# Kernel tuning notes

Hardware: AMD Instinct MI355X
Metric: run time of the kernel (lower is better)

Reference implementation:

```python
import jax, jax.numpy as jnp
import numpy as np

N = 50000
E = 1600000
IN = 128
HID = 128
OUT = 64
NL = 200000
NEG_SLOPE = 0.2


def _glorot(key, shape):
    fan_in, fan_out = shape[0], shape[-1]
    s = jnp.sqrt(6.0 / (fan_in + fan_out))
    return jax.random.uniform(key, shape, jnp.float32, -s, s)


def setup_inputs() -> dict:
    key = jax.random.key(0)
    ks = jax.random.split(key, 16)
    x = jax.random.normal(ks[0], (N, IN), jnp.float32)
    edge_index = jax.random.randint(ks[1], (2, E), 0, N, dtype=jnp.int32)
    edge_label_index = jax.random.randint(ks[2], (2, NL), 0, N, dtype=jnp.int32)
    return {
        "x": x,
        "edge_index": edge_index,
        "edge_label_index": edge_label_index,
        "W1": _glorot(ks[3], (IN, HID)),  "a1s": _glorot(ks[4], (HID,)),  "a1d": _glorot(ks[5], (HID,)),  "b1": jnp.zeros((HID,), jnp.float32),
        "W2": _glorot(ks[6], (HID, HID)), "a2s": _glorot(ks[7], (HID,)),  "a2d": _glorot(ks[8], (HID,)),  "b2": jnp.zeros((HID,), jnp.float32),
        "W3": _glorot(ks[9], (HID, HID)), "a3s": _glorot(ks[10], (HID,)), "a3d": _glorot(ks[11], (HID,)), "b3": jnp.zeros((HID,), jnp.float32),
        "W4": _glorot(ks[12], (HID, OUT)), "b4": jnp.zeros((OUT,), jnp.float32),
    }


def _add_self_loops(edge_index, n):
    loop = jnp.arange(n, dtype=edge_index.dtype)
    return jnp.concatenate([edge_index, jnp.stack([loop, loop])], axis=1)


def gat_conv(x, edge_index, W, a_s, a_d, b):
    """PyG GATConv, heads=1, add_self_loops=True: gather, LeakyReLU score,
    segment softmax over destination nodes, scatter-add aggregate."""
    n = x.shape[0]
    ei = _add_self_loops(edge_index, n)
    src, dst = ei[0], ei[1]
    h = x @ W                                    # [N, H]
    e = jax.nn.leaky_relu((h @ a_s)[src] + (h @ a_d)[dst], NEG_SLOPE)  # [E']
    m = jax.ops.segment_max(e, dst, num_segments=n)
    p = jnp.exp(e - m[dst])
    s = jax.ops.segment_sum(p, dst, num_segments=n)
    alpha = p / s[dst]                           # segment softmax
    out = jax.ops.segment_sum(h[src] * alpha[:, None], dst, num_segments=n)
    return out + b


def gcn_conv(x, edge_index, W, b):
    """PyG GCNConv: self-loops + symmetric degree normalization."""
    n = x.shape[0]
    ei = _add_self_loops(edge_index, n)
    src, dst = ei[0], ei[1]
    h = x @ W
    deg = jax.ops.segment_sum(jnp.ones(src.shape, h.dtype), dst, num_segments=n)
    dinv = jax.lax.rsqrt(deg)
    norm = dinv[src] * dinv[dst]                 # [E']
    out = jax.ops.segment_sum(h[src] * norm[:, None], dst, num_segments=n)
    return out + b


def reference(x, edge_index, edge_label_index,
              W1, a1s, a1d, b1, W2, a2s, a2d, b2,
              W3, a3s, a3d, b3, W4, b4):
    h = jax.nn.relu(gat_conv(x, edge_index, W1, a1s, a1d, b1))
    h = jax.nn.relu(gat_conv(h, edge_index, W2, a2s, a2d, b2))
    h = jax.nn.relu(gat_conv(h, edge_index, W3, a3s, a3d, b3))
    z = gcn_conv(h, edge_index, W4, b4)          # [N, OUT]
    # decode: dot product of endpoint embeddings -> link logits [NL]
    return (z[edge_label_index[0]] * z[edge_label_index[1]]).sum(axis=-1)
```

## Files before the change

### kernel.cpp

```cpp
#include <hip/hip_runtime.h>
#include <hip/hip_fp16.h>
#include <math.h>

#define NN   50000
#define NE   1600000
#define NLBL 200000
#define CAP  80
#define NEG  0.2f
#define NBK  196
#define CAPB 8800
#define CHK  4096
#define GBIN 391

typedef unsigned short u16;
typedef _Float16 half8 __attribute__((ext_vector_type(8)));
typedef float floatx4 __attribute__((ext_vector_type(4)));


__device__ void ph_bin(int blk, const int* __restrict__ ei,
                       int* __restrict__ gcnt, unsigned* __restrict__ bins) {
    __shared__ int cntL[NBK];
    __shared__ int offL[NBK];
    __shared__ int curL[NBK];
    __shared__ int curG[NBK];
    __shared__ unsigned stage[CHK];
    const int tid = threadIdx.x;
    const int e0 = blk * CHK + tid * 16;
    const bool act = (e0 + 15) < NE;

    unsigned pk[16];
    int bb[16];
    if (act) {
#pragma unroll
        for (int g = 0; g < 4; ++g) {
            int4 s4 = *(const int4*)&ei[e0 + g * 4];
            int4 d4 = *(const int4*)&ei[NE + e0 + g * 4];
            int sa[4] = {s4.x, s4.y, s4.z, s4.w};
            int da[4] = {d4.x, d4.y, d4.z, d4.w};
#pragma unroll
            for (int k = 0; k < 4; ++k) {
                int idx = g * 4 + k;
                bb[idx] = da[k] >> 8;
                pk[idx] = (unsigned)sa[k] | ((unsigned)(da[k] & 255) << 16)
                        | ((unsigned)bb[idx] << 24);
            }
        }
    }
    for (int i = tid; i < NBK; i += 256) cntL[i] = 0;
    __syncthreads();
    if (act) {
#pragma unroll
        for (int k = 0; k < 16; ++k) atomicAdd(&cntL[bb[k]], 1);
    }
    __syncthreads();
    if (tid < NBK) {
        int acc = 0;
        for (int i = 0; i < tid; ++i) acc += cntL[i];
        offL[tid] = acc;
        curL[tid] = acc;
    }
    __syncthreads();
    for (int i = tid; i < NBK; i += 256) curG[i] = atomicAdd(&gcnt[i], cntL[i]);
    __syncthreads();
    if (act) {
#pragma unroll
        for (int k = 0; k < 16; ++k) {
            int pos = atomicAdd(&curL[bb[k]], 1);
            stage[pos] = pk[k];
        }
    }
    __syncthreads();
    const int tot = offL[NBK - 1] + cntL[NBK - 1];
    for (int j = tid; j < tot; j += 256) {
        unsigned v = stage[j];
        int b = v >> 24;
        int lr = j - offL[b];
        bins[(size_t)b * CAPB + curG[b] + lr] = v & 0x00FFFFFFu;
    }
}

__global__ __launch_bounds__(256) void k_build(const unsigned* __restrict__ bins,
                                               const int* __restrict__ gcnt,
                                               int* __restrict__ cnt,
                                               u16* __restrict__ csr) {
    __shared__ u16 rows[256 * CAP];
    __shared__ int cur[256];
    const int b = blockIdx.x, tid = threadIdx.x;
    const int d0 = b << 8;
    const int nd = min(256, NN - d0);
    if (tid < nd) { cur[tid] = 1; rows[tid * CAP] = (u16)(d0 + tid); }
    __syncthreads();
    const int n = gcnt[b];
    for (int i = tid; i < n; i += 256) {
        unsigned v = bins[(size_t)b * CAPB + i];
        int s = v & 0xFFFF, dl = (v >> 16) & 0xFF;
        int pos = atomicAdd(&cur[dl], 1);
        if (pos < CAP) rows[dl * CAP + pos] = (u16)s;
    }
    __syncthreads();
    const unsigned* rw = (const unsigned*)rows;
    unsigned* cw = (unsigned*)(csr + (size_t)d0 * CAP);
    const int tot = nd * (CAP / 2);
    for (int i = tid; i < tot; i += 256) cw[i] = rw[i];
    if (tid < nd) cnt[d0 + tid] = cur[tid];
}


__global__ __launch_bounds__(256) void k_pre(const float* __restrict__ W1f,
                                             const float* __restrict__ W2f,
                                             const float* __restrict__ W3f,
                                             const float* __restrict__ W4f,
                                             half8* __restrict__ Wf1,
                                             half8* __restrict__ Wf2,
                                             half8* __restrict__ Wf3,
                                             half8* __restrict__ Wf4,
                                             int* __restrict__ gcnt) {
    if (blockIdx.x == 28) {
        int i = threadIdx.x;
        if (i < NBK) gcnt[i] = 0;
        return;
    }
    int e = blockIdx.x * 256 + threadIdx.x;
    const float* W;
    half8* Wf;
    int nout, le;
    if (e < 2048)      { W = W1f; Wf = Wf1; nout = 128; le = e; }
    else if (e < 4096) { W = W2f; Wf = Wf2; nout = 128; le = e - 2048; }
    else if (e < 6144) { W = W3f; Wf = Wf3; nout = 128; le = e - 4096; }
    else               { W = W4f; Wf = Wf4; nout = 64;  le = e - 6144; }
    int c = le >> 8, rem = le & 255, ks = rem >> 6, lane = rem & 63;
    int n = lane & 15, quad = lane >> 4;
    int col = c * 16 + n, k0 = ks * 32 + quad * 8;
    half8 v;
#pragma unroll
    for (int j = 0; j < 8; ++j) v[j] = (_Float16)W[(size_t)(k0 + j) * nout + col];
    Wf[le] = v;
}


template <int NOUT, bool ATTN, typename TA>
__device__ __forceinline__ void gemm_tile(int gt, int lane,
                                          const TA* __restrict__ A,
                                          const half8* __restrict__ Wf,
                                          __half* __restrict__ C,
                                          const float* __restrict__ a_s,
                                          const float* __restrict__ a_d,
                                          float* __restrict__ asv,
                                          float* __restrict__ adv) {
    constexpr int CT = NOUT / 16;
    const int n = lane & 15, quad = lane >> 4;
    if (gt * 16 >= NN) return;
    const int row = gt * 16 + n;

    half8 a[4];
#pragma unroll
    for (int ks = 0; ks < 4; ++ks) {
        int c128 = ks * 32 + quad * 8;
        if constexpr (sizeof(TA) == 2) {
            a[ks] = *(const half8*)((const _Float16*)A + (size_t)row * 128 + c128);
        } else {
            const float* Ap = (const float*)A + (size_t)row * 128 + c128;
            float4 f0 = *(const float4*)Ap;
            float4 f1 = *(const float4*)(Ap + 4);
            half8 v;
            v[0] = (_Float16)f0.x; v[1] = (_Float16)f0.y; v[2] = (_Float16)f0.z; v[3] = (_Float16)f0.w;
            v[4] = (_Float16)f1.x; v[5] = (_Float16)f1.y; v[6] = (_Float16)f1.z; v[7] = (_Float16)f1.w;
            a[ks] = v;
        }
    }

    floatx4 acc[CT];
#pragma unroll
    for (int c = 0; c < CT; ++c) acc[c] = (floatx4){0.f, 0.f, 0.f, 0.f};
#pragma unroll
    for (int c = 0; c < CT; ++c) {
#pragma unroll
        for (int ks = 0; ks < 4; ++ks) {
            half8 b = Wf[(c * 4 + ks) * 64 + lane];
            acc[c] = __builtin_amdgcn_mfma_f32_16x16x32_f16(b, a[ks], acc[c], 0, 0, 0);
        }
    }

#pragma unroll
    for (int c = 0; c < CT; ++c) {
        __half2 h0 = __floats2half2_rn(acc[c][0], acc[c][1]);
        __half2 h1 = __floats2half2_rn(acc[c][2], acc[c][3]);
        uint2 u;
        __builtin_memcpy(&u.x, &h0, 4);
        __builtin_memcpy(&u.y, &h1, 4);
        int col = c * 16 + quad * 4;
        int pl = col >> 5, off = col & 31;
        *(uint2*)&C[((size_t)pl * NN + row) * 32 + off] = u;
    }

    if (ATTN) {
        float ps = 0.f, pd = 0.f;
#pragma unroll
        for (int c = 0; c < CT; ++c) {
#pragma unroll
            for (int reg = 0; reg < 4; ++reg) {
                float w = acc[c][reg];
                ps = fmaf(w, a_s[c * 16 + quad * 4 + reg], ps);
                pd = fmaf(w, a_d[c * 16 + quad * 4 + reg], pd);
            }
        }
        ps += __shfl_xor(ps, 16); ps += __shfl_xor(ps, 32);
        pd += __shfl_xor(pd, 16); pd += __shfl_xor(pd, 32);
        if (quad == 0) { asv[row] = ps; adv[row] = pd; }
    }
}

__global__ __launch_bounds__(256) void k_bin_gemm1(const int* __restrict__ ei,
                                                   int* __restrict__ gcnt,
                                                   unsigned* __restrict__ bins,
                                                   const float* __restrict__ x,
                                                   const half8* __restrict__ Wf1,
                                                   __half* __restrict__ G,
                                                   const float* __restrict__ a_s,
                                                   const float* __restrict__ a_d,
                                                   float* __restrict__ asv,
                                                   float* __restrict__ adv) {
    if (blockIdx.x < GBIN) { ph_bin(blockIdx.x, ei, gcnt, bins); return; }
    int gt = (blockIdx.x - GBIN) * 4 + (threadIdx.x >> 6);
    gemm_tile<128, true, float>(gt, threadIdx.x & 63, x, Wf1, G, a_s, a_d, asv, adv);
}

template <int NOUT, bool ATTN>
__global__ __launch_bounds__(64) void k_gemm64(const __half* __restrict__ A,
                                               const half8* __restrict__ Wf,
                                               __half* __restrict__ C,
                                               const float* __restrict__ a_s,
                                               const float* __restrict__ a_d,
                                               float* __restrict__ asv,
                                               float* __restrict__ adv) {
    gemm_tile<NOUT, ATTN, __half>(blockIdx.x, threadIdx.x & 63, A, Wf, C,
                                  a_s, a_d, asv, adv);
}


__global__ __launch_bounds__(256) void k_scores(const int* __restrict__ cnt,
                                                const u16* __restrict__ csr,
                                                const float* __restrict__ asv,
                                                const float* __restrict__ adv,
                                                float2* __restrict__ msv) {
    int lane = threadIdx.x & 63, wv = threadIdx.x >> 6;
    int d = blockIdx.x * 4 + wv;
    if (d >= NN) return;
    int deg = cnt[d]; if (deg > CAP) deg = CAP;
    const float advd = adv[d];
    const u16* rowp = csr + (size_t)d * CAP;
    int j0 = lane, j1 = lane + 64;
    float e0 = -INFINITY, e1 = -INFINITY;
    if (j0 < deg) {
        float t = asv[rowp[j0]] + advd;
        e0 = (t >= 0.f) ? t : NEG * t;
    }
    if (j1 < deg) {
        float t = asv[rowp[j1]] + advd;
        e1 = (t >= 0.f) ? t : NEG * t;
    }
    float m = fmaxf(e0, e1);
#pragma unroll
    for (int off = 32; off; off >>= 1) m = fmaxf(m, __shfl_xor(m, off));
    float p0 = (j0 < deg) ? __expf(e0 - m) : 0.f;
    float p1 = (j1 < deg) ? __expf(e1 - m) : 0.f;
    float s = p0 + p1;
#pragma unroll
    for (int off = 32; off; off >>= 1) s += __shfl_xor(s, off);
    if (lane == 0) msv[d] = make_float2(m, 1.f / s);
}

__device__ __forceinline__ void fma_h8v(half8 h, float al, float* acc) {
#pragma unroll
    for (int k = 0; k < 8; ++k) acc[k] = fmaf(al, (float)h[k], acc[k]);
}


__global__ __launch_bounds__(256) void k_gat_agg_sl(const __half* __restrict__ h,
                                                    const int* __restrict__ cnt,
                                                    const u16* __restrict__ csr,
                                                    const float* __restrict__ asv,
                                                    const float* __restrict__ adv,
                                                    const float2* __restrict__ msv,
                                                    const float* __restrict__ bias,
                                                    __half* __restrict__ out) {
    __shared__ float2 metaL[4][4][84];
    int lane = threadIdx.x & 63, wv = threadIdx.x >> 6;
    int sl = blockIdx.x & 3;
    int d0 = (blockIdx.x >> 2) * 16 + wv * 4;
    int sub = lane >> 4;
    int dS = d0 + sub;
    int degS = cnt[dS]; if (degS > CAP) degS = CAP;

    float2* mw = &metaL[wv][0][0];
#pragma unroll
    for (int i = 0; i < 6; ++i) {
        int idx = i * 64 + lane;
        if (idx < 336) mw[idx] = make_float2(0.f, 0.f);
    }

    int mdeg = degS;
    mdeg = max(mdeg, __shfl_xor(mdeg, 16));
    mdeg = max(mdeg, __shfl_xor(mdeg, 32));

    const float advd = adv[dS];
    const float2 mi = msv[dS];
    const u16* rowp = csr + (size_t)dS * CAP;
    int jj = lane & 15;
    for (int j = jj; j < mdeg; j += 16) {
        int s = rowp[j];
        float t = asv[s] + advd;
        float e = (t >= 0.f) ? t : NEG * t;
        float al = __expf(e - mi.x) * mi.y;
        bool ok = j < degS;
        metaL[wv][sub][j] = make_float2(ok ? al : 0.f, __int_as_float(ok ? s : 0));
    }

    int slot = (lane >> 2) & 3, r = lane & 3;
    const _Float16* plane = (const _Float16*)h + (size_t)sl * NN * 32;
    float acc[8];
#pragma unroll
    for (int k = 0; k < 8; ++k) acc[k] = 0.f;
    int trips = (mdeg + 3) >> 2;
    const float2* mrow = &metaL[wv][sub][0];
    for (int t = 0; t < trips; ++t) {
        float2 ms = mrow[t * 4 + slot];
        int sj = __float_as_int(ms.y);
        half8 hv = *(const half8*)(plane + (((sj << 2) + r) << 3));
        fma_h8v(hv, ms.x, acc);
    }
#pragma unroll
    for (int k = 0; k < 8; ++k) {
        acc[k] += __shfl_xor(acc[k], 4);
        acc[k] += __shfl_xor(acc[k], 8);
    }
    if ((lane & 12) == 0) {
        int cb = sl * 32 + r * 8;
        __half2 ho[4];
#pragma unroll
        for (int k = 0; k < 4; ++k) {
            float oa = fmaxf(acc[2 * k]     + bias[cb + 2 * k],     0.f);
            float ob = fmaxf(acc[2 * k + 1] + bias[cb + 2 * k + 1], 0.f);
            ho[k] = __floats2half2_rn(oa, ob);
        }
        uint4 u;
        __builtin_memcpy(&u, &ho[0], 16);
        *(uint4*)&out[(size_t)dS * 128 + cb] = u;
    }
}


__global__ __launch_bounds__(256) void k_gcn_agg_sl(const __half* __restrict__ h,
                                                    const int* __restrict__ cnt,
                                                    const u16* __restrict__ csr,
                                                    const float* __restrict__ bias,
                                                    __half* __restrict__ z) {
    __shared__ float2 metaL[4][4][84];
    int lane = threadIdx.x & 63, wv = threadIdx.x >> 6;
    int sl = blockIdx.x & 1;
    int d0 = (blockIdx.x >> 1) * 16 + wv * 4;
    int sub = lane >> 4;
    int dS = d0 + sub;
    int degc = cnt[dS];
    int degS = degc > CAP ? CAP : degc;

    float2* mw = &metaL[wv][0][0];
#pragma unroll
    for (int i = 0; i < 6; ++i) {
        int idx = i * 64 + lane;
        if (idx < 336) mw[idx] = make_float2(0.f, 0.f);
    }

    int mdeg = degS;
    mdeg = max(mdeg, __shfl_xor(mdeg, 16));
    mdeg = max(mdeg, __shfl_xor(mdeg, 32));

    float did = rsqrtf((float)degc);
    const u16* rowp = csr + (size_t)dS * CAP;
    int jj = lane & 15;
    for (int j = jj; j < mdeg; j += 16) {
        int s = rowp[j];
        float nm = rsqrtf((float)cnt[s]) * did;
        bool ok = j < degS;
        metaL[wv][sub][j] = make_float2(ok ? nm : 0.f, __int_as_float(ok ? s : 0));
    }

    int slot = (lane >> 2) & 3, r = lane & 3;
    const _Float16* plane = (const _Float16*)h + (size_t)sl * NN * 32;
    float acc[8];
#pragma unroll
    for (int k = 0; k < 8; ++k) acc[k] = 0.f;
    int trips = (mdeg + 3) >> 2;
    const float2* mrow = &metaL[wv][sub][0];
    for (int t = 0; t < trips; ++t) {
        float2 ms = mrow[t * 4 + slot];
        int sj = __float_as_int(ms.y);
        half8 hv = *(const half8*)(plane + (((sj << 2) + r) << 3));
        fma_h8v(hv, ms.x, acc);
    }
#pragma unroll
    for (int k = 0; k < 8; ++k) {
        acc[k] += __shfl_xor(acc[k], 4);
        acc[k] += __shfl_xor(acc[k], 8);
    }
    if ((lane & 12) == 0) {
        int cb = sl * 32 + r * 8;
        __half2 ho[4];
#pragma unroll
        for (int k = 0; k < 4; ++k) {
            float oa = acc[2 * k]     + bias[cb + 2 * k];
            float ob = acc[2 * k + 1] + bias[cb + 2 * k + 1];
            ho[k] = __floats2half2_rn(oa, ob);
        }
        uint4 u;
        __builtin_memcpy(&u, &ho[0], 16);
        *(uint4*)&z[(size_t)dS * 64 + cb] = u;
    }
}


__global__ __launch_bounds__(256) void k_decode(const __half* __restrict__ z,
                                                const int* __restrict__ eli,
                                                float* __restrict__ outp) {
    int lane = threadIdx.x & 63, wv = threadIdx.x >> 6;
    int g = lane >> 4, r = lane & 15;
    int idx = (blockIdx.x * 4 + wv) * 4 + g;
    if (idx >= NLBL) return;
    int a = eli[idx], b = eli[NLBL + idx];
    uint2 ua = *(const uint2*)&z[(size_t)a * 64 + r * 4];
    uint2 ub = *(const uint2*)&z[(size_t)b * 64 + r * 4];
    float2 a0 = __half22float2(*(__half2*)&ua.x);
    float2 a1 = __half22float2(*(__half2*)&ua.y);
    float2 b0 = __half22float2(*(__half2*)&ub.x);
    float2 b1 = __half22float2(*(__half2*)&ub.y);
    float v = a0.x * b0.x + a0.y * b0.y + a1.x * b1.x + a1.y * b1.y;
#pragma unroll
    for (int off = 8; off; off >>= 1) v += __shfl_xor(v, off);
    if (r == 0) outp[idx] = v;
}


extern "C" void kernel_launch(void* const* d_in, const int* in_sizes, int n_in,
                              void* d_out, int out_size, void* d_ws, size_t ws_size,
                              hipStream_t stream) {
    const float* x   = (const float*)d_in[0];
    const int*   ei  = (const int*)d_in[1];
    const int*   eli = (const int*)d_in[2];
    const float* W1 = (const float*)d_in[3];
    const float* a1s = (const float*)d_in[4];
    const float* a1d = (const float*)d_in[5];
    const float* b1 = (const float*)d_in[6];
    const float* W2 = (const float*)d_in[7];
    const float* a2s = (const float*)d_in[8];
    const float* a2d = (const float*)d_in[9];
    const float* b2 = (const float*)d_in[10];
    const float* W3 = (const float*)d_in[11];
    const float* a3s = (const float*)d_in[12];
    const float* a3d = (const float*)d_in[13];
    const float* b3 = (const float*)d_in[14];
    const float* W4 = (const float*)d_in[15];
    const float* b4 = (const float*)d_in[16];
    float* outp = (float*)d_out;

    char* p = (char*)d_ws;
    auto alloc = [&](size_t bytes) -> char* {
        char* r = p;
        p += (bytes + 255) & ~(size_t)255;
        return r;
    };
    int*    cnt  = (int*)alloc((size_t)NN * 4);
    u16*    csr  = (u16*)alloc((size_t)NN * CAP * 2);
    int*    gcnt = (int*)alloc((size_t)NBK * 4);
    float*  asvA = (float*)alloc((size_t)NN * 4);
    float*  advA = (float*)alloc((size_t)NN * 4);
    float*  asvB = (float*)alloc((size_t)NN * 4);
    float*  advB = (float*)alloc((size_t)NN * 4);
    float2* msv  = (float2*)alloc((size_t)NN * 8);
    __half* G    = (__half*)alloc((size_t)NN * 128 * 2);
    __half* B    = (__half*)alloc((size_t)NN * 128 * 2);
    __half* zf   = (__half*)alloc((size_t)NN * 64 * 2);
    half8*  Wf1  = (half8*)alloc(2048 * 16);
    half8*  Wf2  = (half8*)alloc(2048 * 16);
    half8*  Wf3  = (half8*)alloc(2048 * 16);
    half8*  Wf4  = (half8*)alloc(1024 * 16);
    unsigned* bins = (unsigned*)alloc((size_t)NBK * CAPB * 4);

    const int gG1   = GBIN + 782;
    const int gGemm = (NN + 15) / 16;
    const int gSc   = (NN + 3) / 4;
    const int gAgg  = (NN / 16) * 4;
    const int gGcn  = (NN / 16) * 2;
    const int gDec  = (NLBL + 15) / 16;

    k_pre<<<29, 256, 0, stream>>>(W1, W2, W3, W4, Wf1, Wf2, Wf3, Wf4, gcnt);
    k_bin_gemm1<<<gG1, 256, 0, stream>>>(ei, gcnt, bins, x, Wf1, G, a1s, a1d, asvA, advA);
    k_build<<<NBK, 256, 0, stream>>>(bins, gcnt, cnt, csr);

    k_scores<<<gSc, 256, 0, stream>>>(cnt, csr, asvA, advA, msv);
    k_gat_agg_sl<<<gAgg, 256, 0, stream>>>(G, cnt, csr, asvA, advA, msv, b1, B);
    k_gemm64<128, true><<<gGemm, 64, 0, stream>>>(B, Wf2, G, a2s, a2d, asvB, advB);

    k_scores<<<gSc, 256, 0, stream>>>(cnt, csr, asvB, advB, msv);
    k_gat_agg_sl<<<gAgg, 256, 0, stream>>>(G, cnt, csr, asvB, advB, msv, b2, B);
    k_gemm64<128, true><<<gGemm, 64, 0, stream>>>(B, Wf3, G, a3s, a3d, asvA, advA);

    k_scores<<<gSc, 256, 0, stream>>>(cnt, csr, asvA, advA, msv);
    k_gat_agg_sl<<<gAgg, 256, 0, stream>>>(G, cnt, csr, asvA, advA, msv, b3, B);
    k_gemm64<64, false><<<gGemm, 64, 0, stream>>>(B, Wf4, G, nullptr, nullptr, nullptr, nullptr);

    k_gcn_agg_sl<<<gGcn, 256, 0, stream>>>(G, cnt, csr, b4, zf);

    k_decode<<<gDec, 256, 0, stream>>>(zf, eli, outp);
}
```

Before: 456.8 us.

## Fuse softmax max/sum into GAT aggregation and replace LDS metadata with shuffles

Removes the separate k_scores kernel by computing the per-destination max and sum of the segment softmax inside the aggregation kernel. Each of 16 lanes holds up to 5 neighbours in registers. The LDS metadata staging is replaced by register shuffles that hand out neighbour indices and weights, and gathers are batched four at a time to raise memory-level parallelism. The GCN aggregation gets the same register and shuffle treatment. This saves three kernel launches and the msv round trip, at the cost of more registers and redundant score computation across the four feature-slice blocks per node.

```diff
diff --git a/kernel.cpp b/kernel.cpp
--- a/kernel.cpp
+++ b/kernel.cpp
@@ -237,39 +237,6 @@
                                   a_s, a_d, asv, adv);
 }
 
-
-__global__ __launch_bounds__(256) void k_scores(const int* __restrict__ cnt,
-                                                const u16* __restrict__ csr,
-                                                const float* __restrict__ asv,
-                                                const float* __restrict__ adv,
-                                                float2* __restrict__ msv) {
-    int lane = threadIdx.x & 63, wv = threadIdx.x >> 6;
-    int d = blockIdx.x * 4 + wv;
-    if (d >= NN) return;
-    int deg = cnt[d]; if (deg > CAP) deg = CAP;
-    const float advd = adv[d];
-    const u16* rowp = csr + (size_t)d * CAP;
-    int j0 = lane, j1 = lane + 64;
-    float e0 = -INFINITY, e1 = -INFINITY;
-    if (j0 < deg) {
-        float t = asv[rowp[j0]] + advd;
-        e0 = (t >= 0.f) ? t : NEG * t;
-    }
-    if (j1 < deg) {
-        float t = asv[rowp[j1]] + advd;
-        e1 = (t >= 0.f) ? t : NEG * t;
-    }
-    float m = fmaxf(e0, e1);
-#pragma unroll
-    for (int off = 32; off; off >>= 1) m = fmaxf(m, __shfl_xor(m, off));
-    float p0 = (j0 < deg) ? __expf(e0 - m) : 0.f;
-    float p1 = (j1 < deg) ? __expf(e1 - m) : 0.f;
-    float s = p0 + p1;
-#pragma unroll
-    for (int off = 32; off; off >>= 1) s += __shfl_xor(s, off);
-    if (lane == 0) msv[d] = make_float2(m, 1.f / s);
-}
-
 __device__ __forceinline__ void fma_h8v(half8 h, float al, float* acc) {
 #pragma unroll
     for (int k = 0; k < 8; ++k) acc[k] = fmaf(al, (float)h[k], acc[k]);
@@ -281,54 +248,83 @@
                                                     const u16* __restrict__ csr,
                                                     const float* __restrict__ asv,
                                                     const float* __restrict__ adv,
-                                                    const float2* __restrict__ msv,
                                                     const float* __restrict__ bias,
                                                     __half* __restrict__ out) {
-    __shared__ float2 metaL[4][4][84];
     int lane = threadIdx.x & 63, wv = threadIdx.x >> 6;
     int sl = blockIdx.x & 3;
     int d0 = (blockIdx.x >> 2) * 16 + wv * 4;
     int sub = lane >> 4;
     int dS = d0 + sub;
     int degS = cnt[dS]; if (degS > CAP) degS = CAP;
-
-    float2* mw = &metaL[wv][0][0];
-#pragma unroll
-    for (int i = 0; i < 6; ++i) {
-        int idx = i * 64 + lane;
-        if (idx < 336) mw[idx] = make_float2(0.f, 0.f);
-    }
+    int jj = lane & 15;
+    const u16* rowp = csr + (size_t)dS * CAP;
+
+    int s0 = rowp[jj];
+    int s1 = rowp[jj + 16];
+    int s2 = rowp[jj + 32];
+    int s3 = rowp[jj + 48];
+    int s4 = rowp[jj + 64];
+    bool v0 = jj < degS, v1 = jj + 16 < degS, v2 = jj + 32 < degS,
+         v3 = jj + 48 < degS, v4 = jj + 64 < degS;
+    s0 = v0 ? s0 : 0; s1 = v1 ? s1 : 0; s2 = v2 ? s2 : 0;
+    s3 = v3 ? s3 : 0; s4 = v4 ? s4 : 0;
+
+    float y0 = asv[s0], y1 = asv[s1], y2 = asv[s2], y3 = asv[s3], y4 = asv[s4];
+    const float advd = adv[dS];
+
+    float t0 = y0 + advd, t1 = y1 + advd, t2 = y2 + advd, t3 = y3 + advd, t4 = y4 + advd;
+    float e0 = v0 ? ((t0 >= 0.f) ? t0 : NEG * t0) : -INFINITY;
+    float e1 = v1 ? ((t1 >= 0.f) ? t1 : NEG * t1) : -INFINITY;
+    float e2 = v2 ? ((t2 >= 0.f) ? t2 : NEG * t2) : -INFINITY;
+    float e3 = v3 ? ((t3 >= 0.f) ? t3 : NEG * t3) : -INFINITY;
+    float e4 = v4 ? ((t4 >= 0.f) ? t4 : NEG * t4) : -INFINITY;
+
+    float m = fmaxf(fmaxf(fmaxf(e0, e1), fmaxf(e2, e3)), e4);
+    m = fmaxf(m, __shfl_xor(m, 1));
+    m = fmaxf(m, __shfl_xor(m, 2));
+    m = fmaxf(m, __shfl_xor(m, 4));
+    m = fmaxf(m, __shfl_xor(m, 8));
+    float p0 = __expf(e0 - m), p1 = __expf(e1 - m), p2 = __expf(e2 - m),
+          p3 = __expf(e3 - m), p4 = __expf(e4 - m);
+    float s = p0 + p1 + p2 + p3 + p4;
+    s += __shfl_xor(s, 1);
+    s += __shfl_xor(s, 2);
+    s += __shfl_xor(s, 4);
+    s += __shfl_xor(s, 8);
+    float inv = 1.f / s;
+    float al0 = p0 * inv, al1 = p1 * inv, al2 = p2 * inv, al3 = p3 * inv, al4 = p4 * inv;
 
     int mdeg = degS;
     mdeg = max(mdeg, __shfl_xor(mdeg, 16));
     mdeg = max(mdeg, __shfl_xor(mdeg, 32));
 
-    const float advd = adv[dS];
-    const float2 mi = msv[dS];
-    const u16* rowp = csr + (size_t)dS * CAP;
-    int jj = lane & 15;
-    for (int j = jj; j < mdeg; j += 16) {
-        int s = rowp[j];
-        float t = asv[s] + advd;
-        float e = (t >= 0.f) ? t : NEG * t;
-        float al = __expf(e - mi.x) * mi.y;
-        bool ok = j < degS;
-        metaL[wv][sub][j] = make_float2(ok ? al : 0.f, __int_as_float(ok ? s : 0));
-    }
-
     int slot = (lane >> 2) & 3, r = lane & 3;
-    const _Float16* plane = (const _Float16*)h + (size_t)sl * NN * 32;
+    const _Float16* plane = (const _Float16*)h + (size_t)sl * NN * 32 + r * 8;
     float acc[8];
 #pragma unroll
     for (int k = 0; k < 8; ++k) acc[k] = 0.f;
-    int trips = (mdeg + 3) >> 2;
-    const float2* mrow = &metaL[wv][sub][0];
-    for (int t = 0; t < trips; ++t) {
-        float2 ms = mrow[t * 4 + slot];
-        int sj = __float_as_int(ms.y);
-        half8 hv = *(const half8*)(plane + (((sj << 2) + r) << 3));
-        fma_h8v(hv, ms.x, acc);
-    }
+    int sbase = lane & 0x30;
+
+    auto chunk = [&](float alK, int sK) {
+        float aa[4]; int ss[4];
+#pragma unroll
+        for (int t2 = 0; t2 < 4; ++t2) {
+            int srcl = sbase | (t2 << 2) | slot;
+            aa[t2] = __shfl(alK, srcl);
+            ss[t2] = __shfl(sK, srcl);
+        }
+        half8 hv[4];
+#pragma unroll
+        for (int t2 = 0; t2 < 4; ++t2) hv[t2] = *(const half8*)(plane + (size_t)ss[t2] * 32);
+#pragma unroll
+        for (int t2 = 0; t2 < 4; ++t2) fma_h8v(hv[t2], aa[t2], acc);
+    };
+    chunk(al0, s0);
+    if (mdeg > 16) chunk(al1, s1);
+    if (mdeg > 32) chunk(al2, s2);
+    if (mdeg > 48) chunk(al3, s3);
+    if (mdeg > 64) chunk(al4, s4);
+
 #pragma unroll
     for (int k = 0; k < 8; ++k) {
         acc[k] += __shfl_xor(acc[k], 4);
@@ -355,7 +351,6 @@
                                                     const u16* __restrict__ csr,
                                                     const float* __restrict__ bias,
                                                     __half* __restrict__ z) {
-    __shared__ float2 metaL[4][4][84];
     int lane = threadIdx.x & 63, wv = threadIdx.x >> 6;
     int sl = blockIdx.x & 1;
     int d0 = (blockIdx.x >> 1) * 16 + wv * 4;
@@ -363,41 +358,59 @@
     int dS = d0 + sub;
     int degc = cnt[dS];
     int degS = degc > CAP ? CAP : degc;
-
-    float2* mw = &metaL[wv][0][0];
-#pragma unroll
-    for (int i = 0; i < 6; ++i) {
-        int idx = i * 64 + lane;
-        if (idx < 336) mw[idx] = make_float2(0.f, 0.f);
-    }
+    int jj = lane & 15;
+    const u16* rowp = csr + (size_t)dS * CAP;
+
+    int s0 = rowp[jj];
+    int s1 = rowp[jj + 16];
+    int s2 = rowp[jj + 32];
+    int s3 = rowp[jj + 48];
+    int s4 = rowp[jj + 64];
+    bool v0 = jj < degS, v1 = jj + 16 < degS, v2 = jj + 32 < degS,
+         v3 = jj + 48 < degS, v4 = jj + 64 < degS;
+    s0 = v0 ? s0 : 0; s1 = v1 ? s1 : 0; s2 = v2 ? s2 : 0;
+    s3 = v3 ? s3 : 0; s4 = v4 ? s4 : 0;
+
+    float c0 = (float)cnt[s0], c1 = (float)cnt[s1], c2 = (float)cnt[s2],
+          c3 = (float)cnt[s3], c4 = (float)cnt[s4];
+    float did = rsqrtf((float)degc);
+    float al0 = v0 ? rsqrtf(c0) * did : 0.f;
+    float al1 = v1 ? rsqrtf(c1) * did : 0.f;
+    float al2 = v2 ? rsqrtf(c2) * did : 0.f;
+    float al3 = v3 ? rsqrtf(c3) * did : 0.f;
+    float al4 = v4 ? rsqrtf(c4) * did : 0.f;
 
     int mdeg = degS;
     mdeg = max(mdeg, __shfl_xor(mdeg, 16));
     mdeg = max(mdeg, __shfl_xor(mdeg, 32));
 
-    float did = rsqrtf((float)degc);
-    const u16* rowp = csr + (size_t)dS * CAP;
-    int jj = lane & 15;
-    for (int j = jj; j < mdeg; j += 16) {
-        int s = rowp[j];
-        float nm = rsqrtf((float)cnt[s]) * did;
-        bool ok = j < degS;
-        metaL[wv][sub][j] = make_float2(ok ? nm : 0.f, __int_as_float(ok ? s : 0));
-    }
-
     int slot = (lane >> 2) & 3, r = lane & 3;
-    const _Float16* plane = (const _Float16*)h + (size_t)sl * NN * 32;
+    const _Float16* plane = (const _Float16*)h + (size_t)sl * NN * 32 + r * 8;
     float acc[8];
 #pragma unroll
     for (int k = 0; k < 8; ++k) acc[k] = 0.f;
-    int trips = (mdeg + 3) >> 2;
-    const float2* mrow = &metaL[wv][sub][0];
-    for (int t = 0; t < trips; ++t) {
-        float2 ms = mrow[t * 4 + slot];
-        int sj = __float_as_int(ms.y);
-        half8 hv = *(const half8*)(plane + (((sj << 2) + r) << 3));
-        fma_h8v(hv, ms.x, acc);
-    }
+    int sbase = lane & 0x30;
+
+    auto chunk = [&](float alK, int sK) {
+        float aa[4]; int ss[4];
+#pragma unroll
+        for (int t2 = 0; t2 < 4; ++t2) {
+            int srcl = sbase | (t2 << 2) | slot;
+            aa[t2] = __shfl(alK, srcl);
+            ss[t2] = __shfl(sK, srcl);
+        }
+        half8 hv[4];
+#pragma unroll
+        for (int t2 = 0; t2 < 4; ++t2) hv[t2] = *(const half8*)(plane + (size_t)ss[t2] * 32);
+#pragma unroll
+        for (int t2 = 0; t2 < 4; ++t2) fma_h8v(hv[t2], aa[t2], acc);
+    };
+    chunk(al0, s0);
+    if (mdeg > 16) chunk(al1, s1);
+    if (mdeg > 32) chunk(al2, s2);
+    if (mdeg > 48) chunk(al3, s3);
+    if (mdeg > 64) chunk(al4, s4);
+
 #pragma unroll
     for (int k = 0; k < 8; ++k) {
         acc[k] += __shfl_xor(acc[k], 4);
@@ -475,7 +488,6 @@
     float*  advA = (float*)alloc((size_t)NN * 4);
     float*  asvB = (float*)alloc((size_t)NN * 4);
     float*  advB = (float*)alloc((size_t)NN * 4);
-    float2* msv  = (float2*)alloc((size_t)NN * 8);
     __half* G    = (__half*)alloc((size_t)NN * 128 * 2);
     __half* B    = (__half*)alloc((size_t)NN * 128 * 2);
     __half* zf   = (__half*)alloc((size_t)NN * 64 * 2);
@@ -487,7 +499,6 @@
 
     const int gG1   = GBIN + 782;
     const int gGemm = (NN + 15) / 16;
-    const int gSc   = (NN + 3) / 4;
     const int gAgg  = (NN / 16) * 4;
     const int gGcn  = (NN / 16) * 2;
     const int gDec  = (NLBL + 15) / 16;
@@ -496,16 +507,13 @@
     k_bin_gemm1<<<gG1, 256, 0, stream>>>(ei, gcnt, bins, x, Wf1, G, a1s, a1d, asvA, advA);
     k_build<<<NBK, 256, 0, stream>>>(bins, gcnt, cnt, csr);
 
-    k_scores<<<gSc, 256, 0, stream>>>(cnt, csr, asvA, advA, msv);
-    k_gat_agg_sl<<<gAgg, 256, 0, stream>>>(G, cnt, csr, asvA, advA, msv, b1, B);
+    k_gat_agg_sl<<<gAgg, 256, 0, stream>>>(G, cnt, csr, asvA, advA, b1, B);
     k_gemm64<128, true><<<gGemm, 64, 0, stream>>>(B, Wf2, G, a2s, a2d, asvB, advB);
 
-    k_scores<<<gSc, 256, 0, stream>>>(cnt, csr, asvB, advB, msv);
-    k_gat_agg_sl<<<gAgg, 256, 0, stream>>>(G, cnt, csr, asvB, advB, msv, b2, B);
+    k_gat_agg_sl<<<gAgg, 256, 0, stream>>>(G, cnt, csr, asvB, advB, b2, B);
     k_gemm64<128, true><<<gGemm, 64, 0, stream>>>(B, Wf3, G, a3s, a3d, asvA, advA);
 
-    k_scores<<<gSc, 256, 0, stream>>>(cnt, csr, asvA, advA, msv);
-    k_gat_agg_sl<<<gAgg, 256, 0, stream>>>(G, cnt, csr, asvA, advA, msv, b3, B);
+    k_gat_agg_sl<<<gAgg, 256, 0, stream>>>(G, cnt, csr, asvA, advA, b3, B);
     k_gemm64<64, false><<<gGemm, 64, 0, stream>>>(B, Wf4, G, nullptr, nullptr, nullptr, nullptr);
 
     k_gcn_agg_sl<<<gGcn, 256, 0, stream>>>(G, cnt, csr, b4, zf);
```

After: 403.5 us. 11.7% less time.
